# Optimization experiments

Measured on AMD Instinct MI355X. Metric: run time of the kernel, lower is better.

## Reference

```python
import jax, jax.numpy as jnp
import numpy as np

THETAS = np.linspace(0.5, 1.5, 9)


def _interp_nearest(x, theta):
    # torch F.interpolate(mode='nearest') on last dim: src = floor(dst * in/out)
    in_len = x.shape[-1]
    out_len = int(np.floor(in_len * theta))
    idx = np.floor(np.arange(out_len) * (in_len / out_len)).astype(np.int32)
    return x[..., idx]


def _argaug(x, y):
    # x, y: (B, T, idim)
    B, T, idim_q = y.shape
    pad = idim_q - 1
    sim_max_global = jnp.zeros((B, T), x.dtype)
    x_aug = None
    for theta in THETAS:
        x_s = _interp_nearest(x, float(theta))          # (B, T, idim_k)
        idim_k = x_s.shape[-1]
        key_pad = jnp.pad(x_s, ((0, 0), (0, 0), (pad, pad)))
        n_shift = idim_k + idim_q - 1
        win_idx = np.arange(n_shift)[:, None] + np.arange(idim_q)[None, :]  # (S, q)
        trunk = key_pad[:, :, win_idx]                  # (B, T, S, q)
        denom = jnp.linalg.norm(y, axis=-1)[..., None] * jnp.linalg.norm(trunk, axis=-1)
        sim = jnp.einsum('btq,btsq->bts', y, trunk) / denom  # (B, T, S)
        sim_max = jnp.max(sim, axis=-1)
        sim_idx = jnp.argmax(sim, axis=-1)              # (B, T) int
        x_shift = jnp.take_along_axis(trunk, sim_idx[..., None, None], axis=2)[:, :, 0, :]
        mask = sim_max_global < sim_max
        sim_max_global = jnp.where(mask, sim_max, sim_max_global)
        if x_aug is None:
            x_aug = x_shift
        else:
            x_aug = jnp.where(mask[..., None], x_shift, x_aug)
    return x_aug, sim_max_global


def setup_inputs() -> dict:
    key = jax.random.key(0)
    ks = jax.random.split(key, 4)
    B, T, idim, hdim, odim = 4, 256, 256, 1024, 256
    x = jax.random.normal(ks[0], (B, T, idim), jnp.float32)
    y = jax.random.normal(ks[1], (B, T, odim), jnp.float32)
    W1 = jax.random.normal(ks[2], (idim, hdim), jnp.float32) * (1.0 / np.sqrt(idim))
    b1 = jnp.zeros((hdim,), jnp.float32)
    W2 = jax.random.normal(ks[3], (hdim, odim), jnp.float32) * (1.0 / np.sqrt(hdim))
    b2 = jnp.zeros((odim,), jnp.float32)
    # hg kernel: gaussian over hidden index, normalized to max 1 -> P(mask==1)
    w = np.exp(-0.5 * (np.arange(hdim, dtype=np.float32) / 430.0) ** 2)
    freq = jnp.asarray(w / w.max(), jnp.float32)
    return {"x": x, "y": y, "W1": W1, "b1": b1, "W2": W2, "b2": b2, "freq": freq}


def reference(x, y, W1, b1, W2, b2, freq):
    ignore_out = 0.0
    x_aug, _ = _argaug(x, y)                 # (B, T, idim)
    idim = x.shape[-1]
    odim = y.shape[-1]
    xf = x_aug.reshape(-1, idim)             # (N, idim)
    yf = y.reshape(-1, odim)                 # (N, odim)
    hdim = W1.shape[1]
    # freq_mask: multinomial over (1-w, w) per hidden unit == bernoulli(w)
    mk = jax.random.bernoulli(jax.random.key(42), freq, (xf.shape[0], hdim))
    h = (xf @ W1 + b1) * mk.astype(xf.dtype)
    out = h @ W2 + b2 + xf                   # (N, odim)
    # NetLoss: masked elementwise MSE, mean over non-ignored entries
    m = yf == ignore_out
    denom = (~m).astype(xf.dtype).sum()
    loss = jnp.where(m, 0.0, (out - yf) ** 2).sum() / denom
    return loss, out
```

## Files before the change

### kernel.cpp

```cpp
#include <hip/hip_runtime.h>
#include <stdint.h>

#define ROWS 1024
#define IDIM 256
#define HDIM 1024

__device__ __forceinline__ uint32_t rotl32(uint32_t x, int r){ return (x<<r)|(x>>(32-r)); }

__device__ __forceinline__ void threefry(uint32_t x0, uint32_t x1, uint32_t& o0, uint32_t& o1){
  const uint32_t k0 = 0u, k1 = 42u;
  const uint32_t k2 = 0x1BD11BDAu ^ k0 ^ k1;
  x0 += k0; x1 += k1;
#define TFR(r) { x0 += x1; x1 = rotl32(x1, r); x1 ^= x0; }
  TFR(13) TFR(15) TFR(26) TFR(6)  x0 += k1; x1 += k2 + 1u;
  TFR(17) TFR(29) TFR(16) TFR(24) x0 += k2; x1 += k0 + 2u;
  TFR(13) TFR(15) TFR(26) TFR(6)  x0 += k0; x1 += k1 + 3u;
  TFR(17) TFR(29) TFR(16) TFR(24) x0 += k1; x1 += k2 + 4u;
  TFR(13) TFR(15) TFR(26) TFR(6)  x0 += k2; x1 += k0 + 5u;
#undef TFR
  o0 = x0; o1 = x1;
}

__global__ __launch_bounds__(256) void mask_kernel(const float* __restrict__ freq,
                                                   float* __restrict__ mkf)
{
  uint32_t i = blockIdx.x * 256u + threadIdx.x;
  uint32_t o0, o1;
  threefry(0u, i, o0, o1);
  uint32_t bits = o0 ^ o1;
  float u = __uint_as_float((bits >> 9) | 0x3F800000u) - 1.0f;
  mkf[i] = (u < freq[i & 1023u]) ? 1.0f : 0.0f;
}

__global__ __launch_bounds__(256) void argaug_kernel(const float* __restrict__ x,
                                                     const float* __restrict__ y,
                                                     float* __restrict__ xaug)
{
  __shared__ float  xs[IDIM];
  __shared__ float  ys[IDIM];
  __shared__ float  kp[1024];
  __shared__ double rv[256];
  __shared__ int    rk[256];

  const int row  = blockIdx.x;
  const int tid  = threadIdx.x;
  const int wave = tid >> 6;
  const int lane = tid & 63;

  xs[tid] = x[row * IDIM + tid];
  ys[tid] = y[row * IDIM + tid];
  __syncthreads();

  double bestv = -1.0e300; int bestk = 0x3FFFFFFF;
  double t0v   = -1.0e300; int t0k   = 0x3FFFFFFF;
  const int sbase = 192 * wave + 3 * lane;

  for (int t = 0; t < 9; ++t) {
    const int OL = 128 + 32 * t;
    const double ratio = 256.0 / (double)OL;

    for (int i = tid; i < 1024; i += 256) {
      float v = 0.0f;
      int j = i - 255;
      if (j >= 0 && j < OL) v = xs[(int)floor((double)j * ratio)];
      kp[i] = v;
    }
    __syncthreads();

    double a0=0,a1=0,a2=0, n0=0,n1=0,n2=0;
    const int qlo = (wave == 0) ? 64 : 0;
    const int qhi = min(256, 255 + OL - 192 * wave);
    if (qhi > qlo) {
      int p = sbase + qlo;
      double c0 = (double)kp[p], c1 = (double)kp[p+1], c2 = (double)kp[p+2], c3;
      for (int q = qlo; q < qhi; q += 4) {
        float4 y4 = *(const float4*)&ys[q];
        double yd = (double)y4.x;
        a0 += yd*c0; n0 += c0*c0;
        a1 += yd*c1; n1 += c1*c1;
        a2 += yd*c2; n2 += c2*c2;
        c3 = (double)kp[p+3];
        yd = (double)y4.y;
        a0 += yd*c1; n0 += c1*c1;
        a1 += yd*c2; n1 += c2*c2;
        a2 += yd*c3; n2 += c3*c3;
        c0 = (double)kp[p+4];
        yd = (double)y4.z;
        a0 += yd*c2; n0 += c2*c2;
        a1 += yd*c3; n1 += c3*c3;
        a2 += yd*c0; n2 += c0*c0;
        c1 = (double)kp[p+5];
        yd = (double)y4.w;
        a0 += yd*c3; n0 += c3*c3;
        a1 += yd*c0; n1 += c0*c0;
        a2 += yd*c1; n2 += c1*c1;
        c2 = (double)kp[p+6];
        p += 4;
      }
    }

    const int nsh = OL + 255;
#define UPD(S, A, N) { int s = (S); if (s < nsh && (N) > 0.0) { double v = (A) / sqrt((N)); \
      if (v > bestv) { bestv = v; bestk = (t << 10) | s; } \
      if (t == 0 && v > t0v) { t0v = v; t0k = s; } } }
    UPD(sbase,     a0, n0)
    UPD(sbase + 1, a1, n1)
    UPD(sbase + 2, a2, n2)
#undef UPD
    __syncthreads();
  }

  rv[tid] = bestv; rk[tid] = bestk;
  __syncthreads();
  for (int off = 128; off > 0; off >>= 1) {
    if (tid < off) {
      double v2 = rv[tid+off]; int k2 = rk[tid+off];
      if (v2 > rv[tid] || (v2 == rv[tid] && k2 < rk[tid])) { rv[tid] = v2; rk[tid] = k2; }
    }
    __syncthreads();
  }
  const double gbest = rv[0];
  const int    gk    = rk[0];
  __syncthreads();

  rv[tid] = t0v; rk[tid] = t0k;
  __syncthreads();
  for (int off = 128; off > 0; off >>= 1) {
    if (tid < off) {
      double v2 = rv[tid+off]; int k2 = rk[tid+off];
      if (v2 > rv[tid] || (v2 == rv[tid] && k2 < rk[tid])) { rv[tid] = v2; rk[tid] = k2; }
    }
    __syncthreads();
  }
  const int wk = (gbest > 0.0) ? gk : rk[0];

  const int tb = wk >> 10, sb = wk & 1023;
  const int OLb = 128 + 32 * tb;
  const double ratiob = 256.0 / (double)OLb;
  int j = sb + tid - 255;
  float v = 0.0f;
  if (j >= 0 && j < OLb) v = xs[(int)floor((double)j * ratiob)];
  xaug[row * IDIM + tid] = v;
}

__global__ __launch_bounds__(256) void gemm1_kernel(const float* __restrict__ A,
                                                    const float* __restrict__ W1,
                                                    const float* __restrict__ b1,
                                                    const float* __restrict__ mkf,
                                                    float* __restrict__ h)
{
  __shared__ float As[32][68];
  __shared__ float Bs[32][68];
  const int tid = threadIdx.x;
  const int m0 = blockIdx.x * 64;
  const int n0 = blockIdx.y * 64;
  const int tx = tid & 15, ty = tid >> 4;
  float acc[4][4] = {};

  for (int kt = 0; kt < 256; kt += 32) {
#pragma unroll
    for (int jj = 0; jj < 8; ++jj) {
      int f = tid + 256*jj;
      As[f & 31][f >> 5] = A[(m0 + (f >> 5)) * 256 + kt + (f & 31)];
    }
#pragma unroll
    for (int jj = 0; jj < 8; ++jj) {
      int f = tid + 256*jj;
      Bs[f >> 6][f & 63] = W1[(kt + (f >> 6)) * 1024 + n0 + (f & 63)];
    }
    __syncthreads();
#pragma unroll
    for (int kk = 0; kk < 32; ++kk) {
      float4 a4 = *(const float4*)&As[kk][4*ty];
      float4 b4 = *(const float4*)&Bs[kk][4*tx];
      acc[0][0] += a4.x*b4.x; acc[0][1] += a4.x*b4.y; acc[0][2] += a4.x*b4.z; acc[0][3] += a4.x*b4.w;
      acc[1][0] += a4.y*b4.x; acc[1][1] += a4.y*b4.y; acc[1][2] += a4.y*b4.z; acc[1][3] += a4.y*b4.w;
      acc[2][0] += a4.z*b4.x; acc[2][1] += a4.z*b4.y; acc[2][2] += a4.z*b4.z; acc[2][3] += a4.z*b4.w;
      acc[3][0] += a4.w*b4.x; acc[3][1] += a4.w*b4.y; acc[3][2] += a4.w*b4.z; acc[3][3] += a4.w*b4.w;
    }
    __syncthreads();
  }

  float4 bias = *(const float4*)&b1[n0 + 4*tx];
#pragma unroll
  for (int r = 0; r < 4; ++r) {
    int m = m0 + 4*ty + r;
    float4 mk4 = *(const float4*)&mkf[m * 1024 + n0 + 4*tx];
    float4 o;
    o.x = (acc[r][0] + bias.x) * mk4.x;
    o.y = (acc[r][1] + bias.y) * mk4.y;
    o.z = (acc[r][2] + bias.z) * mk4.z;
    o.w = (acc[r][3] + bias.w) * mk4.w;
    *(float4*)&h[m * 1024 + n0 + 4*tx] = o;
  }
}

__global__ __launch_bounds__(256) void gemm2_kernel(const float* __restrict__ h,
                                                    const float* __restrict__ W2,
                                                    float* __restrict__ out_acc)
{
  __shared__ float As[32][68];
  __shared__ float Bs[32][68];
  const int tid = threadIdx.x;
  const int m0 = blockIdx.x * 64;
  const int n0 = blockIdx.y * 64;
  const int kz = blockIdx.z * 256;
  const int tx = tid & 15, ty = tid >> 4;
  float acc[4][4] = {};

  for (int kt = 0; kt < 256; kt += 32) {
#pragma unroll
    for (int jj = 0; jj < 8; ++jj) {
      int f = tid + 256*jj;
      As[f & 31][f >> 5] = h[(m0 + (f >> 5)) * 1024 + kz + kt + (f & 31)];
    }
#pragma unroll
    for (int jj = 0; jj < 8; ++jj) {
      int f = tid + 256*jj;
      Bs[f >> 6][f & 63] = W2[(kz + kt + (f >> 6)) * 256 + n0 + (f & 63)];
    }
    __syncthreads();
#pragma unroll
    for (int kk = 0; kk < 32; ++kk) {
      float4 a4 = *(const float4*)&As[kk][4*ty];
      float4 b4 = *(const float4*)&Bs[kk][4*tx];
      acc[0][0] += a4.x*b4.x; acc[0][1] += a4.x*b4.y; acc[0][2] += a4.x*b4.z; acc[0][3] += a4.x*b4.w;
      acc[1][0] += a4.y*b4.x; acc[1][1] += a4.y*b4.y; acc[1][2] += a4.y*b4.z; acc[1][3] += a4.y*b4.w;
      acc[2][0] += a4.z*b4.x; acc[2][1] += a4.z*b4.y; acc[2][2] += a4.z*b4.z; acc[2][3] += a4.z*b4.w;
      acc[3][0] += a4.w*b4.x; acc[3][1] += a4.w*b4.y; acc[3][2] += a4.w*b4.z; acc[3][3] += a4.w*b4.w;
    }
    __syncthreads();
  }

#pragma unroll
  for (int r = 0; r < 4; ++r)
#pragma unroll
    for (int c = 0; c < 4; ++c)
      unsafeAtomicAdd(&out_acc[(m0 + 4*ty + r) * 256 + n0 + 4*tx + c], acc[r][c]);
}

__global__ __launch_bounds__(256) void finalize_kernel(const float* __restrict__ out_acc,
                                                       const float* __restrict__ b2,
                                                       const float* __restrict__ xaug,
                                                       const float* __restrict__ yref,
                                                       float* __restrict__ d_out,
                                                       double* __restrict__ loss_acc,
                                                       unsigned int* __restrict__ cnt_acc)
{
  __shared__ double sred[4];
  __shared__ unsigned int cred[4];
  int i = blockIdx.x * 256 + threadIdx.x;
  int n = i & 255;
  float v = out_acc[i] + b2[n] + xaug[i];
  d_out[1 + i] = v;
  float yv = yref[i];
  bool valid = (yv != 0.0f);
  float df = v - yv;
  double lsd = valid ? (double)df * (double)df : 0.0;
#pragma unroll
  for (int off = 32; off > 0; off >>= 1) lsd += __shfl_down(lsd, off, 64);
  unsigned long long bal = __ballot(valid);
  int wv = threadIdx.x >> 6, ln = threadIdx.x & 63;
  if (ln == 0) { sred[wv] = lsd; cred[wv] = (unsigned int)__popcll(bal); }
  __syncthreads();
  if (threadIdx.x == 0) {
    double s = sred[0] + sred[1] + sred[2] + sred[3];
    unsigned int c = cred[0] + cred[1] + cred[2] + cred[3];
    atomicAdd(loss_acc, s);
    atomicAdd(cnt_acc, c);
  }
}

__global__ void loss_kernel(const double* __restrict__ loss_acc,
                            const unsigned int* __restrict__ cnt_acc,
                            float* __restrict__ d_out)
{
  d_out[0] = (float)(loss_acc[0] / (double)cnt_acc[0]);
}

extern "C" void kernel_launch(void* const* d_in, const int* in_sizes, int n_in,
                              void* d_out, int out_size, void* d_ws, size_t ws_size,
                              hipStream_t stream) {
  const float* x    = (const float*)d_in[0];
  const float* y    = (const float*)d_in[1];
  const float* W1   = (const float*)d_in[2];
  const float* b1   = (const float*)d_in[3];
  const float* W2   = (const float*)d_in[4];
  const float* b2   = (const float*)d_in[5];
  const float* freq = (const float*)d_in[6];
  float* out = (float*)d_out;

  char* ws = (char*)d_ws;
  float*  xaug = (float*)(ws);
  float*  h    = (float*)(ws + (1u<<20));
  float*  mkf  = (float*)(ws + 5u*(1u<<20));
  float*  oacc = (float*)(ws + 9u*(1u<<20));
  double* lacc = (double*)(ws + 10u*(1u<<20));
  unsigned int* cacc = (unsigned int*)(ws + 10u*(1u<<20) + 8u);

  hipMemsetAsync(ws + 9u*(1u<<20), 0, (1u<<20) + 16u, stream);

  mask_kernel  <<<4096, 256, 0, stream>>>(freq, mkf);
  argaug_kernel<<<1024, 256, 0, stream>>>(x, y, xaug);
  gemm1_kernel <<<dim3(16,16),  256, 0, stream>>>(xaug, W1, b1, mkf, h);
  gemm2_kernel <<<dim3(16,4,4), 256, 0, stream>>>(h, W2, oacc);
  finalize_kernel<<<1024, 256, 0, stream>>>(oacc, b2, xaug, y, out, lacc, cacc);
  loss_kernel  <<<1, 1, 0, stream>>>(lacc, cacc, out);
}
```

Before: 274.7 us.

## Score argaug shifts in fp32 with prefix-sum norms, then rescore candidates in fp64

```diff
diff --git a/kernel.cpp b/kernel.cpp
--- a/kernel.cpp
+++ b/kernel.cpp
@@ -39,26 +39,30 @@
   __shared__ float  xs[IDIM];
   __shared__ float  ys[IDIM];
   __shared__ float  kp[1024];
+  __shared__ double P[1025];
+  __shared__ float  vst[5888];
   __shared__ double rv[256];
   __shared__ int    rk[256];
-
-  const int row  = blockIdx.x;
+  __shared__ double wv[4];
+  __shared__ int    cnt;
+  __shared__ int    list[128];
+
   const int tid  = threadIdx.x;
   const int wave = tid >> 6;
   const int lane = tid & 63;
+  const int row  = blockIdx.x;
 
   xs[tid] = x[row * IDIM + tid];
   ys[tid] = y[row * IDIM + tid];
-  __syncthreads();
-
-  double bestv = -1.0e300; int bestk = 0x3FFFFFFF;
-  double t0v   = -1.0e300; int t0k   = 0x3FFFFFFF;
+#pragma unroll
+  for (int i = tid; i < 5888; i += 256) vst[i] = -1.0e30f;
   const int sbase = 192 * wave + 3 * lane;
 
   for (int t = 0; t < 9; ++t) {
     const int OL = 128 + 32 * t;
     const double ratio = 256.0 / (double)OL;
 
+    __syncthreads();
     for (int i = tid; i < 1024; i += 256) {
       float v = 0.0f;
       int j = i - 255;
@@ -67,50 +71,120 @@
     }
     __syncthreads();
 
-    double a0=0,a1=0,a2=0, n0=0,n1=0,n2=0;
+    {
+      double d0 = (double)kp[4*tid+0]; d0 *= d0;
+      double d1 = (double)kp[4*tid+1]; d1 *= d1;
+      double d2 = (double)kp[4*tid+2]; d2 *= d2;
+      double d3 = (double)kp[4*tid+3]; d3 *= d3;
+      double p1 = d0, p2 = p1 + d1, p3 = p2 + d2, p4 = p3 + d3;
+      double sc = p4;
+#pragma unroll
+      for (int d = 1; d < 64; d <<= 1) {
+        double u = __shfl_up(sc, d, 64);
+        if (lane >= d) sc += u;
+      }
+      if (lane == 63) wv[wave] = sc;
+      __syncthreads();
+      double wo = 0.0;
+      if (wave > 0) wo += wv[0];
+      if (wave > 1) wo += wv[1];
+      if (wave > 2) wo += wv[2];
+      double excl = wo + (sc - p4);
+      P[4*tid+1] = excl + p1; P[4*tid+2] = excl + p2;
+      P[4*tid+3] = excl + p3; P[4*tid+4] = excl + p4;
+      if (tid == 0) P[0] = 0.0;
+      __syncthreads();
+    }
+
+    float a0 = 0.f, a1 = 0.f, a2 = 0.f;
     const int qlo = (wave == 0) ? 64 : 0;
     const int qhi = min(256, 255 + OL - 192 * wave);
     if (qhi > qlo) {
       int p = sbase + qlo;
-      double c0 = (double)kp[p], c1 = (double)kp[p+1], c2 = (double)kp[p+2], c3;
+      float c0 = kp[p], c1 = kp[p+1], c2 = kp[p+2], c3;
       for (int q = qlo; q < qhi; q += 4) {
         float4 y4 = *(const float4*)&ys[q];
-        double yd = (double)y4.x;
-        a0 += yd*c0; n0 += c0*c0;
-        a1 += yd*c1; n1 += c1*c1;
-        a2 += yd*c2; n2 += c2*c2;
-        c3 = (double)kp[p+3];
-        yd = (double)y4.y;
-        a0 += yd*c1; n0 += c1*c1;
-        a1 += yd*c2; n1 += c2*c2;
-        a2 += yd*c3; n2 += c3*c3;
-        c0 = (double)kp[p+4];
-        yd = (double)y4.z;
-        a0 += yd*c2; n0 += c2*c2;
-        a1 += yd*c3; n1 += c3*c3;
-        a2 += yd*c0; n2 += c0*c0;
-        c1 = (double)kp[p+5];
-        yd = (double)y4.w;
-        a0 += yd*c3; n0 += c3*c3;
-        a1 += yd*c0; n1 += c0*c0;
-        a2 += yd*c1; n2 += c1*c1;
-        c2 = (double)kp[p+6];
+        a0 += y4.x*c0; a1 += y4.x*c1; a2 += y4.x*c2;
+        c3 = kp[p+3];
+        a0 += y4.y*c1; a1 += y4.y*c2; a2 += y4.y*c3;
+        c0 = kp[p+4];
+        a0 += y4.z*c2; a1 += y4.z*c3; a2 += y4.z*c0;
+        c1 = kp[p+5];
+        a0 += y4.w*c3; a1 += y4.w*c0; a2 += y4.w*c1;
+        c2 = kp[p+6];
         p += 4;
       }
     }
-
     const int nsh = OL + 255;
-#define UPD(S, A, N) { int s = (S); if (s < nsh && (N) > 0.0) { double v = (A) / sqrt((N)); \
-      if (v > bestv) { bestv = v; bestk = (t << 10) | s; } \
-      if (t == 0 && v > t0v) { t0v = v; t0k = s; } } }
-    UPD(sbase,     a0, n0)
-    UPD(sbase + 1, a1, n1)
-    UPD(sbase + 2, a2, n2)
-#undef UPD
-    __syncthreads();
-  }
-
-  rv[tid] = bestv; rk[tid] = bestk;
+#pragma unroll
+    for (int r = 0; r < 3; ++r) {
+      int s = sbase + r;
+      if (s < nsh) {
+        float a = (r == 0) ? a0 : (r == 1) ? a1 : a2;
+        float nf = (float)(P[s+256] - P[s]);
+        if (nf > 0.f) vst[t*640 + s] = a / sqrtf(nf);
+      }
+    }
+  }
+  __syncthreads();
+
+  {
+    float gm = -1.0e30f;
+    for (int i = tid; i < 5888; i += 256) gm = fmaxf(gm, vst[i]);
+    rv[tid] = (double)gm;
+    __syncthreads();
+    for (int off = 128; off > 0; off >>= 1) {
+      if (tid < off) rv[tid] = fmax(rv[tid], rv[tid+off]);
+      __syncthreads();
+    }
+  }
+  const float gmax32 = (float)rv[0];
+  __syncthreads();
+  {
+    float tm = -1.0e30f;
+    for (int i = tid; i < 640; i += 256) tm = fmaxf(tm, vst[i]);
+    rv[tid] = (double)tm;
+    __syncthreads();
+    for (int off = 128; off > 0; off >>= 1) {
+      if (tid < off) rv[tid] = fmax(rv[tid], rv[tid+off]);
+      __syncthreads();
+    }
+  }
+  const float t0max32 = (float)rv[0];
+
+  if (tid == 0) cnt = 0;
+  __syncthreads();
+  const float gthr = gmax32 - 1.0e-3f;
+  const float tthr = t0max32 - 1.0e-3f;
+  for (int i = tid; i < 5888; i += 256) {
+    float v = vst[i];
+    if (v >= gthr || (i < 640 && v >= tthr)) {
+      int id = atomicAdd(&cnt, 1);
+      if (id < 128) list[id] = i;
+    }
+  }
+  __syncthreads();
+  const int m = min(cnt, 128);
+
+  double v64 = -1.0e300; int key = 0x3FFFFFFF;
+  if (tid < m) {
+    int slot = list[tid];
+    int tt = slot / 640;
+    int ss = slot - tt * 640;
+    int OLr = 128 + 32 * tt;
+    double ratior = 256.0 / (double)OLr;
+    double a64 = 0.0, n64 = 0.0;
+    for (int q = 0; q < 256; ++q) {
+      int j = ss + q - 255;
+      double c = 0.0;
+      if (j >= 0 && j < OLr) c = (double)xs[(int)floor((double)j * ratior)];
+      a64 += (double)ys[q] * c;
+      n64 += c * c;
+    }
+    if (n64 > 0.0) { v64 = a64 / sqrt(n64); key = (tt << 10) | ss; }
+  }
+
+  rv[tid] = v64; rk[tid] = key;
   __syncthreads();
   for (int off = 128; off > 0; off >>= 1) {
     if (tid < off) {
@@ -123,7 +197,8 @@
   const int    gk    = rk[0];
   __syncthreads();
 
-  rv[tid] = t0v; rk[tid] = t0k;
+  rv[tid] = ((key >> 10) == 0) ? v64 : -1.0e300;
+  rk[tid] = key;
   __syncthreads();
   for (int off = 128; off > 0; off >>= 1) {
     if (tid < off) {
@@ -184,14 +259,14 @@
   float4 bias = *(const float4*)&b1[n0 + 4*tx];
 #pragma unroll
   for (int r = 0; r < 4; ++r) {
-    int m = m0 + 4*ty + r;
-    float4 mk4 = *(const float4*)&mkf[m * 1024 + n0 + 4*tx];
+    int mm = m0 + 4*ty + r;
+    float4 mk4 = *(const float4*)&mkf[mm * 1024 + n0 + 4*tx];
     float4 o;
     o.x = (acc[r][0] + bias.x) * mk4.x;
     o.y = (acc[r][1] + bias.y) * mk4.y;
     o.z = (acc[r][2] + bias.z) * mk4.z;
     o.w = (acc[r][3] + bias.w) * mk4.w;
-    *(float4*)&h[m * 1024 + n0 + 4*tx] = o;
+    *(float4*)&h[mm * 1024 + n0 + 4*tx] = o;
   }
 }
 
@@ -260,8 +335,8 @@
 #pragma unroll
   for (int off = 32; off > 0; off >>= 1) lsd += __shfl_down(lsd, off, 64);
   unsigned long long bal = __ballot(valid);
-  int wv = threadIdx.x >> 6, ln = threadIdx.x & 63;
-  if (ln == 0) { sred[wv] = lsd; cred[wv] = (unsigned int)__popcll(bal); }
+  int wvx = threadIdx.x >> 6, ln = threadIdx.x & 63;
+  if (ln == 0) { sred[wvx] = lsd; cred[wvx] = (unsigned int)__popcll(bal); }
   __syncthreads();
   if (threadIdx.x == 0) {
     double s = sred[0] + sred[1] + sred[2] + sred[3];
```

Result: slower. 318.5 us (+15.9%).
